# Kernel optimization log

Measured on AMD Instinct MI355X. Metric: run time of the kernel, lower is better.

## Reference

```python
import jax, jax.numpy as jnp
import numpy as np

HIDDEN = 1024
NUM_EXPERTS = 8
TOP_K = 2
INNER = HIDDEN * 2
B, S = 4, 2048


def setup_inputs() -> dict:
    key = jax.random.key(0)
    ks = jax.random.split(key, 8)
    sd = 1.0 / np.sqrt(HIDDEN)
    si = 1.0 / np.sqrt(INNER)
    return {
        "x": jax.random.normal(ks[0], (B, S, HIDDEN), dtype=jnp.float32),
        "Wr": jax.random.uniform(ks[1], (HIDDEN, NUM_EXPERTS), jnp.float32, -sd, sd),
        "br": jax.random.uniform(ks[2], (NUM_EXPERTS,), jnp.float32, -sd, sd),
        "W1": jax.random.uniform(ks[3], (NUM_EXPERTS, HIDDEN, INNER), jnp.float32, -sd, sd),
        "b1": jax.random.uniform(ks[4], (NUM_EXPERTS, INNER), jnp.float32, -sd, sd),
        "W2": jax.random.uniform(ks[5], (NUM_EXPERTS, INNER, HIDDEN), jnp.float32, -si, si),
        "b2": jax.random.uniform(ks[6], (NUM_EXPERTS, HIDDEN), jnp.float32, -si, si),
    }


def reference(x, Wr, br, W1, b1, W2, b2):
    batch, seq, hidden = x.shape
    tokens = x.reshape(-1, hidden)                       # [N, d]
    n = tokens.shape[0]
    logits = tokens @ Wr + br                            # [N, E]
    top_w, top_i = jax.lax.top_k(logits, TOP_K)          # [N, k]
    top_w = jax.nn.softmax(top_w, axis=-1)
    # Dense per-token expert weights (zero outside top-k) — equivalent to the
    # sorted-dispatch + index_add combine in the original.
    weights = jnp.zeros((n, NUM_EXPERTS), dtype=top_w.dtype)
    weights = weights.at[jnp.arange(n)[:, None], top_i].add(top_w)  # [N, E]
    out = jnp.zeros_like(tokens)
    for e in range(NUM_EXPERTS):  # fixed small loop over experts
        h = jax.nn.relu(tokens @ W1[e] + b1[e])          # [N, inner]
        y = h @ W2[e] + b2[e]                            # [N, d]
        out = out + y * weights[:, e:e + 1]
    return out.reshape(batch, seq, hidden)
```

## Files before the change

### kernel.cpp

```cpp
#include <hip/hip_runtime.h>
#include <stdint.h>

#define HID    1024
#define EXPERTS 8
#define TOPK   2
#define INNER  2048
#define NTOK   8192
#define NPAIR  (NTOK * TOPK)
#define MAXT   136

#define BM 128
#define BN 128
#define BK 32

typedef _Float16 f16;
typedef f16   f16x8 __attribute__((ext_vector_type(8)));
typedef float f32x4 __attribute__((ext_vector_type(4)));

__device__ __forceinline__ void gload_lds16(const void* g, void* l) {
  __builtin_amdgcn_global_load_lds(
      (const __attribute__((address_space(1))) void*)g,
      (__attribute__((address_space(3))) void*)l, 16, 0, 0);
}

__global__ void router_kernel(const float* __restrict__ x,
                              const float* __restrict__ Wr,
                              const float* __restrict__ br,
                              int* __restrict__ e_sel, float* __restrict__ w_sel) {
  int gid  = blockIdx.x * blockDim.x + threadIdx.x;
  int wid  = gid >> 6;
  int lane = gid & 63;
  if (wid >= NTOK) return;

  const f32x4* xr = (const f32x4*)(x + (size_t)wid * HID);
  float acc[EXPERTS];
#pragma unroll
  for (int e = 0; e < EXPERTS; ++e) acc[e] = 0.f;

#pragma unroll
  for (int j = 0; j < HID / 256; ++j) {
    f32x4 xv = xr[j * 64 + lane];
    int   k  = (j * 64 + lane) * 4;
    const float* wr = Wr + (size_t)k * EXPERTS;
#pragma unroll
    for (int r = 0; r < 4; ++r) {
      float xs = xv[r];
      f32x4 w0 = *(const f32x4*)(wr + r * 8);
      f32x4 w1 = *(const f32x4*)(wr + r * 8 + 4);
#pragma unroll
      for (int e = 0; e < 4; ++e) { acc[e] += xs * w0[e]; acc[4 + e] += xs * w1[e]; }
    }
  }
#pragma unroll
  for (int e = 0; e < EXPERTS; ++e) {
#pragma unroll
    for (int off = 32; off > 0; off >>= 1) acc[e] += __shfl_xor(acc[e], off);
  }
  if (lane == 0) {
    float lg[EXPERTS];
#pragma unroll
    for (int e = 0; e < EXPERTS; ++e) lg[e] = acc[e] + br[e];
    int e0 = 0; float l0 = lg[0];
#pragma unroll
    for (int e = 1; e < EXPERTS; ++e) if (lg[e] > l0) { l0 = lg[e]; e0 = e; }
    int e1 = -1; float l1 = -3.4e38f;
#pragma unroll
    for (int e = 0; e < EXPERTS; ++e) if (e != e0 && lg[e] > l1) { l1 = lg[e]; e1 = e; }
    float a  = __expf(l1 - l0);
    float w0 = 1.f / (1.f + a);
    float w1 = a * w0;
    e_sel[wid * 2]     = e0;  e_sel[wid * 2 + 1] = e1;
    w_sel[wid * 2]     = w0;  w_sel[wid * 2 + 1] = w1;
  }
}

__global__ __launch_bounds__(1024) void dispatch_kernel(
    const int* __restrict__ e_sel, const float* __restrict__ w_sel,
    int* __restrict__ tok_list, float* __restrict__ wt_list,
    int* __restrict__ counts, int* __restrict__ bases,
    int* __restrict__ tile_e, int* __restrict__ tile_m0,
    int* __restrict__ tinfo) {
  __shared__ int scnt[EXPERTS][1024];
  __shared__ int etot[EXPERTS];
  __shared__ int ebase[EXPERTS];
  int tid = threadIdx.x, lane = tid & 63, wv = tid >> 6;

  int myE[16]; float myW[16];
  int lc[EXPERTS];
#pragma unroll
  for (int e = 0; e < EXPERTS; ++e) lc[e] = 0;
#pragma unroll
  for (int i = 0; i < 16; ++i) {
    int p = tid * 16 + i;
    myE[i] = e_sel[p];
    myW[i] = w_sel[p];
#pragma unroll
    for (int e = 0; e < EXPERTS; ++e) lc[e] += (myE[i] == e);
  }
#pragma unroll
  for (int e = 0; e < EXPERTS; ++e) scnt[e][tid] = lc[e];
  __syncthreads();

  if (wv < EXPERTS) {
    int run = 0;
    for (int c = 0; c < 16; ++c) {
      int v = scnt[wv][c * 64 + lane];
      int incl = v;
#pragma unroll
      for (int off = 1; off < 64; off <<= 1) {
        int n = __shfl_up(incl, off);
        if (lane >= off) incl += n;
      }
      scnt[wv][c * 64 + lane] = run + incl - v;
      run += __shfl(incl, 63);
    }
    if (lane == 0) etot[wv] = run;
  }
  __syncthreads();

  if (tid == 0) {
    int s = 0, t = 0;
    for (int e = 0; e < EXPERTS; ++e) {
      ebase[e] = s; bases[e] = s; counts[e] = etot[e];
      for (int m0 = 0; m0 < etot[e]; m0 += BM) { tile_e[t] = e; tile_m0[t] = m0; ++t; }
      s += etot[e];
    }
    tinfo[0] = t;
  }
  __syncthreads();

  int cur[EXPERTS];
#pragma unroll
  for (int e = 0; e < EXPERTS; ++e) cur[e] = ebase[e] + scnt[e][tid];
#pragma unroll
  for (int i = 0; i < 16; ++i) {
    int p = 0;
#pragma unroll
    for (int e = 0; e < EXPERTS; ++e) if (myE[i] == e) p = cur[e]++;
    tok_list[p] = (tid * 16 + i) >> 1;
    wt_list[p]  = myW[i];
  }
}

__global__ void convert_x_kernel(const float* __restrict__ x,
                                 f16* __restrict__ x16, int n8) {
  int i = blockIdx.x * blockDim.x + threadIdx.x;
  int stride = gridDim.x * blockDim.x;
  for (; i < n8; i += stride) {
    f32x4 a = ((const f32x4*)x)[i * 2];
    f32x4 b = ((const f32x4*)x)[i * 2 + 1];
    f16x8 o;
#pragma unroll
    for (int j = 0; j < 4; ++j) { o[j] = (f16)a[j]; o[4 + j] = (f16)b[j]; }
    ((f16x8*)x16)[i] = o;
  }
}

__global__ void transpose_cvt_kernel(const float* __restrict__ src,
                                     f16* __restrict__ dst, int R, int C) {
  __shared__ float tile[32][33];
  int z = blockIdx.z;
  src += (size_t)z * R * C;
  dst += (size_t)z * R * C;
  int c0 = blockIdx.x * 32, r0 = blockIdx.y * 32;
  int tx = threadIdx.x, ty = threadIdx.y;
#pragma unroll
  for (int i = 0; i < 4; ++i)
    tile[ty + i * 8][tx] = src[(size_t)(r0 + ty + i * 8) * C + c0 + tx];
  __syncthreads();
#pragma unroll
  for (int i = 0; i < 4; ++i)
    dst[(size_t)(c0 + ty + i * 8) * R + r0 + tx] = (f16)tile[tx][ty + i * 8];
}

__global__ __launch_bounds__(256) void gemm1_kernel(
    const f16* __restrict__ x16, const f16* __restrict__ w1t,
    const float* __restrict__ b1, const int* __restrict__ tok_list,
    const int* __restrict__ counts, const int* __restrict__ bases,
    const int* __restrict__ tile_e, const int* __restrict__ tile_m0,
    const int* __restrict__ tinfo, int c0,
    f16* __restrict__ h16) {
  int g = blockIdx.y;
  int t = c0 + g;
  if (t >= tinfo[0]) return;
  int e    = tile_e[t];
  int m0   = tile_m0[t];
  int cnt  = counts[e];
  int base = bases[e];
  int n0   = blockIdx.x * BN;
  const f16* Bg = w1t + (size_t)e * INNER * HID;

  __shared__ f16 As[BM * BK];
  __shared__ f16 Bs[BN * BK];

  int tid = threadIdx.x;
  int lane = tid & 63, wid = tid >> 6;
  int wm = (wid >> 1) * 64, wn = (wid & 1) * 64;

  int rA0  = tid >> 2, rA1 = 64 + (tid >> 2);
  int koff = (tid & 3) * 8;
  int tok0 = tok_list[base + min(m0 + rA0, cnt - 1)];
  int tok1 = tok_list[base + min(m0 + rA1, cnt - 1)];
  const f16* gA0 = x16 + (size_t)tok0 * HID + koff;
  const f16* gA1 = x16 + (size_t)tok1 * HID + koff;
  const f16* gB0 = Bg + (size_t)(n0 + rA0) * HID + koff;
  const f16* gB1 = Bg + (size_t)(n0 + rA1) * HID + koff;

  f16* lA0 = As + wid * 512;
  f16* lA1 = As + 2048 + wid * 512;
  f16* lB0 = Bs + wid * 512;
  f16* lB1 = Bs + 2048 + wid * 512;

  f32x4 acc[4][4];
#pragma unroll
  for (int i = 0; i < 4; ++i)
#pragma unroll
    for (int j = 0; j < 4; ++j) acc[i][j] = (f32x4){0.f, 0.f, 0.f, 0.f};

  int ar = lane & 15;
  int ko = (lane >> 4) * 8;

  for (int ks = 0; ks < HID / BK; ++ks) {
    __syncthreads();
    gload_lds16(gA0, lA0); gload_lds16(gA1, lA1);
    gload_lds16(gB0, lB0); gload_lds16(gB1, lB1);
    gA0 += BK; gA1 += BK; gB0 += BK; gB1 += BK;
    __syncthreads();

    f16x8 a[4], b[4];
#pragma unroll
    for (int mi = 0; mi < 4; ++mi)
      a[mi] = *(const f16x8*)(As + (wm + mi * 16 + ar) * BK + ko);
#pragma unroll
    for (int ni = 0; ni < 4; ++ni)
      b[ni] = *(const f16x8*)(Bs + (wn + ni * 16 + ar) * BK + ko);
#pragma unroll
    for (int mi = 0; mi < 4; ++mi)
#pragma unroll
      for (int ni = 0; ni < 4; ++ni)
        acc[mi][ni] = __builtin_amdgcn_mfma_f32_16x16x32_f16(a[mi], b[ni], acc[mi][ni], 0, 0, 0);
  }

  int col = lane & 15, rb = (lane >> 4) * 4;
  float bb[4];
#pragma unroll
  for (int ni = 0; ni < 4; ++ni) bb[ni] = b1[e * INNER + n0 + wn + ni * 16 + col];
#pragma unroll
  for (int mi = 0; mi < 4; ++mi)
#pragma unroll
    for (int r = 0; r < 4; ++r) {
      int ml = wm + mi * 16 + rb + r;
      if (m0 + ml < cnt) {
        size_t rowoff = (size_t)(g * BM + ml) * INNER + n0 + wn + col;
#pragma unroll
        for (int ni = 0; ni < 4; ++ni) {
          float v = acc[mi][ni][r] + bb[ni];
          h16[rowoff + ni * 16] = (f16)fmaxf(v, 0.f);
        }
      }
    }
}

__global__ __launch_bounds__(256) void gemm2_kernel(
    const f16* __restrict__ h16, const f16* __restrict__ w2t,
    const float* __restrict__ b2, const int* __restrict__ tok_list,
    const float* __restrict__ wt_list, const int* __restrict__ counts,
    const int* __restrict__ bases,
    const int* __restrict__ tile_e, const int* __restrict__ tile_m0,
    const int* __restrict__ tinfo, int c0,
    float* __restrict__ out) {
  int g = blockIdx.y;
  int t = c0 + g;
  if (t >= tinfo[0]) return;
  int e    = tile_e[t];
  int m0   = tile_m0[t];
  int cnt  = counts[e];
  int base = bases[e];
  int d0   = blockIdx.x * BN;
  const f16* Bg = w2t + (size_t)e * HID * INNER;

  __shared__ f16 As[BM * BK];
  __shared__ f16 Bs[BN * BK];

  int tid = threadIdx.x;
  int lane = tid & 63, wid = tid >> 6;
  int wm = (wid >> 1) * 64, wn = (wid & 1) * 64;

  int rA0  = tid >> 2, rA1 = 64 + (tid >> 2);
  int koff = (tid & 3) * 8;
  int lm0 = min(m0 + rA0, cnt - 1) - m0;
  int lm1 = min(m0 + rA1, cnt - 1) - m0;
  const f16* gA0 = h16 + (size_t)(g * BM + lm0) * INNER + koff;
  const f16* gA1 = h16 + (size_t)(g * BM + lm1) * INNER + koff;
  const f16* gB0 = Bg + (size_t)(d0 + rA0) * INNER + koff;
  const f16* gB1 = Bg + (size_t)(d0 + rA1) * INNER + koff;

  f16* lA0 = As + wid * 512;
  f16* lA1 = As + 2048 + wid * 512;
  f16* lB0 = Bs + wid * 512;
  f16* lB1 = Bs + 2048 + wid * 512;

  f32x4 acc[4][4];
#pragma unroll
  for (int i = 0; i < 4; ++i)
#pragma unroll
    for (int j = 0; j < 4; ++j) acc[i][j] = (f32x4){0.f, 0.f, 0.f, 0.f};

  int ar = lane & 15;
  int ko = (lane >> 4) * 8;

  for (int ks = 0; ks < INNER / BK; ++ks) {
    __syncthreads();
    gload_lds16(gA0, lA0); gload_lds16(gA1, lA1);
    gload_lds16(gB0, lB0); gload_lds16(gB1, lB1);
    gA0 += BK; gA1 += BK; gB0 += BK; gB1 += BK;
    __syncthreads();

    f16x8 a[4], b[4];
#pragma unroll
    for (int mi = 0; mi < 4; ++mi)
      a[mi] = *(const f16x8*)(As + (wm + mi * 16 + ar) * BK + ko);
#pragma unroll
    for (int ni = 0; ni < 4; ++ni)
      b[ni] = *(const f16x8*)(Bs + (wn + ni * 16 + ar) * BK + ko);
#pragma unroll
    for (int mi = 0; mi < 4; ++mi)
#pragma unroll
      for (int ni = 0; ni < 4; ++ni)
        acc[mi][ni] = __builtin_amdgcn_mfma_f32_16x16x32_f16(a[mi], b[ni], acc[mi][ni], 0, 0, 0);
  }

  int col = lane & 15, rb = (lane >> 4) * 4;
  float bb[4];
#pragma unroll
  for (int ni = 0; ni < 4; ++ni) bb[ni] = b2[e * HID + d0 + wn + ni * 16 + col];
#pragma unroll
  for (int mi = 0; mi < 4; ++mi)
#pragma unroll
    for (int r = 0; r < 4; ++r) {
      int ml = wm + mi * 16 + rb + r;
      if (m0 + ml < cnt) {
        int   p   = base + m0 + ml;
        int   tok = tok_list[p];
        float w   = wt_list[p];
        float* orow = out + (size_t)tok * HID + d0 + wn + col;
#pragma unroll
        for (int ni = 0; ni < 4; ++ni) {
          float v = acc[mi][ni][r] + bb[ni];
          atomicAdd(orow + ni * 16, v * w);
        }
      }
    }
}

extern "C" void kernel_launch(void* const* d_in, const int* in_sizes, int n_in,
                              void* d_out, int out_size, void* d_ws, size_t ws_size,
                              hipStream_t stream) {
  (void)in_sizes; (void)n_in;
  const float* x  = (const float*)d_in[0];
  const float* Wr = (const float*)d_in[1];
  const float* br = (const float*)d_in[2];
  const float* W1 = (const float*)d_in[3];
  const float* b1 = (const float*)d_in[4];
  const float* W2 = (const float*)d_in[5];
  const float* b2 = (const float*)d_in[6];
  float* out = (float*)d_out;

  char*  ws  = (char*)d_ws;
  size_t off = 0;
  auto alloc = [&](size_t bytes) {
    char* p = ws + off;
    off += bytes; off = (off + 255) & ~(size_t)255;
    return p;
  };
  int*   tok_list = (int*)alloc(NPAIR * sizeof(int));
  float* wt_list  = (float*)alloc(NPAIR * sizeof(float));
  int*   e_sel    = (int*)alloc(NTOK * 2 * sizeof(int));
  float* w_sel    = (float*)alloc(NTOK * 2 * sizeof(float));
  int*   counts   = (int*)alloc(EXPERTS * sizeof(int));
  int*   bases    = (int*)alloc(EXPERTS * sizeof(int));
  int*   tile_e   = (int*)alloc(MAXT * sizeof(int));
  int*   tile_m0  = (int*)alloc(MAXT * sizeof(int));
  int*   tinfo    = (int*)alloc(16 * sizeof(int));
  f16*   w1t      = (f16*)alloc((size_t)EXPERTS * HID * INNER * sizeof(f16));
  f16*   w2t      = (f16*)alloc((size_t)EXPERTS * HID * INNER * sizeof(f16));
  f16*   x16      = (f16*)alloc((size_t)NTOK * HID * sizeof(f16));
  const size_t TILE_BYTES = (size_t)BM * INNER * sizeof(f16);
  size_t rem = (ws_size > off) ? (ws_size - off) : 0;
  int G = (int)(rem / TILE_BYTES);
  if (G < 1) G = 1;
  if (G > MAXT) G = MAXT;
  int nch = (MAXT + G - 1) / G;
  f16* h16 = (f16*)(ws + off);

  hipMemsetAsync(out, 0, (size_t)out_size * sizeof(float), stream);

  convert_x_kernel<<<2048, 256, 0, stream>>>(x, x16, NTOK * HID / 8);
  transpose_cvt_kernel<<<dim3(INNER / 32, HID / 32, EXPERTS), dim3(32, 8), 0, stream>>>(
      W1, w1t, HID, INNER);
  transpose_cvt_kernel<<<dim3(HID / 32, INNER / 32, EXPERTS), dim3(32, 8), 0, stream>>>(
      W2, w2t, INNER, HID);
  router_kernel<<<NTOK / 4, 256, 0, stream>>>(x, Wr, br, e_sel, w_sel);
  dispatch_kernel<<<1, 1024, 0, stream>>>(e_sel, w_sel, tok_list, wt_list,
                                          counts, bases, tile_e, tile_m0, tinfo);

  for (int c = 0; c < nch; ++c) {
    int c0 = c * G;
    int gy = (MAXT - c0 < G) ? (MAXT - c0) : G;
    gemm1_kernel<<<dim3(INNER / BN, gy, 1), 256, 0, stream>>>(
        x16, w1t, b1, tok_list, counts, bases, tile_e, tile_m0, tinfo, c0, h16);
    gemm2_kernel<<<dim3(HID / BN, gy, 1), 256, 0, stream>>>(
        h16, w2t, b2, tok_list, wt_list, counts, bases, tile_e, tile_m0, tinfo, c0, out);
  }
}
```

Baseline: 506.8 us.

## Double-buffer LDS with BK=64 and XOR-swizzled layout in expert GEMMs

Both expert GEMM kernels now use a K tile of 64 with two ping-pong LDS buffers, so the direct global-to-LDS loads for the next tile are issued while MFMAs run on the current one. The LDS layout is XOR-swizzled by row to avoid bank conflicts on the wider rows, and the number of barriers per K element is halved. The cost is four times the LDS per block (64 KB), which may lower occupancy.

```diff
diff --git a/kernel.cpp b/kernel.cpp
--- a/kernel.cpp
+++ b/kernel.cpp
@@ -11,7 +11,7 @@
 
 #define BM 128
 #define BN 128
-#define BK 32
+#define BK 64
 
 typedef _Float16 f16;
 typedef f16   f16x8 __attribute__((ext_vector_type(8)));
@@ -172,6 +172,30 @@
   for (int i = 0; i < 4; ++i)
     dst[(size_t)(c0 + ty + i * 8) * R + r0 + tx] = (f16)tile[tx][ty + i * 8];
 }
+
+
+#define GEMM_STAGE(AS, BS) do {                                   \
+  _Pragma("unroll") for (int i_ = 0; i_ < 4; ++i_) {              \
+    gload_lds16(gA[i_], &(AS)[i_ * 2048 + wid * 512]);            \
+    gload_lds16(gB[i_], &(BS)[i_ * 2048 + wid * 512]);            \
+    gA[i_] += BK; gB[i_] += BK;                                   \
+  }                                                               \
+} while (0)
+
+#define GEMM_COMPUTE(AS, BS) do {                                               \
+  _Pragma("unroll") for (int kk_ = 0; kk_ < 2; ++kk_) {                         \
+    int cko_ = kk_ ? colk1 : colk0;                                             \
+    f16x8 af_[4], bf_[4];                                                       \
+    _Pragma("unroll") for (int mi_ = 0; mi_ < 4; ++mi_)                         \
+      af_[mi_] = *(const f16x8*)&(AS)[(wm + mi_ * 16 + ar) * 64 + cko_];        \
+    _Pragma("unroll") for (int ni_ = 0; ni_ < 4; ++ni_)                         \
+      bf_[ni_] = *(const f16x8*)&(BS)[(wn + ni_ * 16 + ar) * 64 + cko_];        \
+    _Pragma("unroll") for (int mi_ = 0; mi_ < 4; ++mi_)                         \
+      _Pragma("unroll") for (int ni_ = 0; ni_ < 4; ++ni_)                       \
+        acc[mi_][ni_] = __builtin_amdgcn_mfma_f32_16x16x32_f16(                 \
+            af_[mi_], bf_[ni_], acc[mi_][ni_], 0, 0, 0);                        \
+  }                                                                             \
+} while (0)
 
 __global__ __launch_bounds__(256) void gemm1_kernel(
     const f16* __restrict__ x16, const f16* __restrict__ w1t,
@@ -190,26 +214,24 @@
   int n0   = blockIdx.x * BN;
   const f16* Bg = w1t + (size_t)e * INNER * HID;
 
-  __shared__ f16 As[BM * BK];
-  __shared__ f16 Bs[BN * BK];
+  __shared__ f16 As0[BM * BK], As1[BM * BK];
+  __shared__ f16 Bs0[BM * BK], Bs1[BM * BK];
 
   int tid = threadIdx.x;
   int lane = tid & 63, wid = tid >> 6;
   int wm = (wid >> 1) * 64, wn = (wid & 1) * 64;
 
-  int rA0  = tid >> 2, rA1 = 64 + (tid >> 2);
-  int koff = (tid & 3) * 8;
-  int tok0 = tok_list[base + min(m0 + rA0, cnt - 1)];
-  int tok1 = tok_list[base + min(m0 + rA1, cnt - 1)];
-  const f16* gA0 = x16 + (size_t)tok0 * HID + koff;
-  const f16* gA1 = x16 + (size_t)tok1 * HID + koff;
-  const f16* gB0 = Bg + (size_t)(n0 + rA0) * HID + koff;
-  const f16* gB1 = Bg + (size_t)(n0 + rA1) * HID + koff;
-
-  f16* lA0 = As + wid * 512;
-  f16* lA1 = As + 2048 + wid * 512;
-  f16* lB0 = Bs + wid * 512;
-  f16* lB1 = Bs + 2048 + wid * 512;
+  int trow = tid >> 3;
+  int gcol = (tid & 7) ^ (trow & 7);
+  const f16* gA[4];
+  const f16* gB[4];
+#pragma unroll
+  for (int i = 0; i < 4; ++i) {
+    int row = i * 32 + trow;
+    int tok = tok_list[base + min(m0 + row, cnt - 1)];
+    gA[i] = x16 + (size_t)tok * HID + gcol * 8;
+    gB[i] = Bg + (size_t)(n0 + row) * HID + gcol * 8;
+  }
 
   f32x4 acc[4][4];
 #pragma unroll
@@ -217,31 +239,23 @@
 #pragma unroll
     for (int j = 0; j < 4; ++j) acc[i][j] = (f32x4){0.f, 0.f, 0.f, 0.f};
 
-  int ar = lane & 15;
-  int ko = (lane >> 4) * 8;
-
-  for (int ks = 0; ks < HID / BK; ++ks) {
+  int ar = lane & 15, hi = lane >> 4;
+  int sa = ar & 7;
+  int colk0 = ((hi) ^ sa) * 8;
+  int colk1 = ((4 + hi) ^ sa) * 8;
+
+  GEMM_STAGE(As0, Bs0);
+  __syncthreads();
+  for (int ks = 0; ks < HID / BK; ks += 2) {
+    GEMM_STAGE(As1, Bs1);
+    GEMM_COMPUTE(As0, Bs0);
     __syncthreads();
-    gload_lds16(gA0, lA0); gload_lds16(gA1, lA1);
-    gload_lds16(gB0, lB0); gload_lds16(gB1, lB1);
-    gA0 += BK; gA1 += BK; gB0 += BK; gB1 += BK;
+    if (ks + 2 < HID / BK) GEMM_STAGE(As0, Bs0);
+    GEMM_COMPUTE(As1, Bs1);
     __syncthreads();
-
-    f16x8 a[4], b[4];
-#pragma unroll
-    for (int mi = 0; mi < 4; ++mi)
-      a[mi] = *(const f16x8*)(As + (wm + mi * 16 + ar) * BK + ko);
-#pragma unroll
-    for (int ni = 0; ni < 4; ++ni)
-      b[ni] = *(const f16x8*)(Bs + (wn + ni * 16 + ar) * BK + ko);
-#pragma unroll
-    for (int mi = 0; mi < 4; ++mi)
-#pragma unroll
-      for (int ni = 0; ni < 4; ++ni)
-        acc[mi][ni] = __builtin_amdgcn_mfma_f32_16x16x32_f16(a[mi], b[ni], acc[mi][ni], 0, 0, 0);
-  }
-
-  int col = lane & 15, rb = (lane >> 4) * 4;
+  }
+
+  int col = lane & 15, rb = hi * 4;
   float bb[4];
 #pragma unroll
   for (int ni = 0; ni < 4; ++ni) bb[ni] = b1[e * INNER + n0 + wn + ni * 16 + col];
@@ -279,26 +293,24 @@
   int d0   = blockIdx.x * BN;
   const f16* Bg = w2t + (size_t)e * HID * INNER;
 
-  __shared__ f16 As[BM * BK];
-  __shared__ f16 Bs[BN * BK];
+  __shared__ f16 As0[BM * BK], As1[BM * BK];
+  __shared__ f16 Bs0[BM * BK], Bs1[BM * BK];
 
   int tid = threadIdx.x;
   int lane = tid & 63, wid = tid >> 6;
   int wm = (wid >> 1) * 64, wn = (wid & 1) * 64;
 
-  int rA0  = tid >> 2, rA1 = 64 + (tid >> 2);
-  int koff = (tid & 3) * 8;
-  int lm0 = min(m0 + rA0, cnt - 1) - m0;
-  int lm1 = min(m0 + rA1, cnt - 1) - m0;
-  const f16* gA0 = h16 + (size_t)(g * BM + lm0) * INNER + koff;
-  const f16* gA1 = h16 + (size_t)(g * BM + lm1) * INNER + koff;
-  const f16* gB0 = Bg + (size_t)(d0 + rA0) * INNER + koff;
-  const f16* gB1 = Bg + (size_t)(d0 + rA1) * INNER + koff;
-
-  f16* lA0 = As + wid * 512;
-  f16* lA1 = As + 2048 + wid * 512;
-  f16* lB0 = Bs + wid * 512;
-  f16* lB1 = Bs + 2048 + wid * 512;
+  int trow = tid >> 3;
+  int gcol = (tid & 7) ^ (trow & 7);
+  const f16* gA[4];
+  const f16* gB[4];
+#pragma unroll
+  for (int i = 0; i < 4; ++i) {
+    int row  = i * 32 + trow;
+    int lrow = min(m0 + row, cnt - 1) - m0;
+    gA[i] = h16 + (size_t)(g * BM + lrow) * INNER + gcol * 8;
+    gB[i] = Bg + (size_t)(d0 + row) * INNER + gcol * 8;
+  }
 
   f32x4 acc[4][4];
 #pragma unroll
@@ -306,31 +318,23 @@
 #pragma unroll
     for (int j = 0; j < 4; ++j) acc[i][j] = (f32x4){0.f, 0.f, 0.f, 0.f};
 
-  int ar = lane & 15;
-  int ko = (lane >> 4) * 8;
-
-  for (int ks = 0; ks < INNER / BK; ++ks) {
+  int ar = lane & 15, hi = lane >> 4;
+  int sa = ar & 7;
+  int colk0 = ((hi) ^ sa) * 8;
+  int colk1 = ((4 + hi) ^ sa) * 8;
+
+  GEMM_STAGE(As0, Bs0);
+  __syncthreads();
+  for (int ks = 0; ks < INNER / BK; ks += 2) {
+    GEMM_STAGE(As1, Bs1);
+    GEMM_COMPUTE(As0, Bs0);
     __syncthreads();
-    gload_lds16(gA0, lA0); gload_lds16(gA1, lA1);
-    gload_lds16(gB0, lB0); gload_lds16(gB1, lB1);
-    gA0 += BK; gA1 += BK; gB0 += BK; gB1 += BK;
+    if (ks + 2 < INNER / BK) GEMM_STAGE(As0, Bs0);
+    GEMM_COMPUTE(As1, Bs1);
     __syncthreads();
-
-    f16x8 a[4], b[4];
-#pragma unroll
-    for (int mi = 0; mi < 4; ++mi)
-      a[mi] = *(const f16x8*)(As + (wm + mi * 16 + ar) * BK + ko);
-#pragma unroll
-    for (int ni = 0; ni < 4; ++ni)
-      b[ni] = *(const f16x8*)(Bs + (wn + ni * 16 + ar) * BK + ko);
-#pragma unroll
-    for (int mi = 0; mi < 4; ++mi)
-#pragma unroll
-      for (int ni = 0; ni < 4; ++ni)
-        acc[mi][ni] = __builtin_amdgcn_mfma_f32_16x16x32_f16(a[mi], b[ni], acc[mi][ni], 0, 0, 0);
-  }
-
-  int col = lane & 15, rb = (lane >> 4) * 4;
+  }
+
+  int col = lane & 15, rb = hi * 4;
   float bb[4];
 #pragma unroll
   for (int ni = 0; ni < 4; ++ni) bb[ni] = b2[e * HID + d0 + wn + ni * 16 + col];
```

New measurement: 520.9 us. 1.03x slower.
